# Kernel optimization log

Measured on AMD Instinct MI355X. Metric: run time of the kernel, lower is better.

## Reference

```python
import jax, jax.numpy as jnp
import numpy as np

N, D, E = 16384, 256, 131072  # nodes, feature dim, directed edges (avg sym degree ~16)


def _build_graph(rng):
    # random edges with no self-loops
    r = rng.integers(0, N, E)
    c = (r + 1 + rng.integers(0, N - 1, E)) % N
    e = np.stack([r, c], 1)
    # symmetrize + dedupe + sort == torch sparse coalesce()
    e = np.unique(np.concatenate([e, e[:, ::-1]], 0), axis=0)
    rows, cols = e[:, 0], e[:, 1]
    deg = np.bincount(rows, minlength=N)
    max_deg = int(deg.max())
    off = np.concatenate([[0], np.cumsum(deg)])
    pos = np.arange(rows.shape[0]) - off[rows]
    nbr = np.zeros((N, max_deg), dtype=np.int32)  # padded neighbor lists (CSR rows)
    nbr[rows, pos] = cols
    return nbr, deg.astype(np.int32)


def setup_inputs() -> dict:
    rng = np.random.default_rng(0)
    vertices = jnp.asarray(rng.standard_normal((N, D)).astype(np.float32))
    nbr, deg = _build_graph(rng)
    return {"vertices": vertices, "nbr": jnp.asarray(nbr), "deg": jnp.asarray(deg)}


def _compute_means(vertices, nbr, deg):
    # Sequential greedy edge-based vertex averaging (RelEdgePool phase 1).
    n, d = vertices.shape
    max_deg = nbr.shape[1]
    slot = jnp.arange(max_deg)

    def step(carry, xs):
        unproc, out, c = carry
        i, nbrs_i, deg_i = xs
        valid = slot < deg_i                      # real (non-pad) neighbors
        sel = valid & unproc[nbrs_i]              # unprocessed cluster members (excl. self)
        is_head = unproc[i]                       # vertex starts a new valid cluster
        # mean over unprocessed members; self is always included when head
        s = jnp.einsum('kd,k->d', vertices[nbrs_i], sel.astype(vertices.dtype)) + vertices[i]
        cnt = (jnp.sum(sel) + 1).astype(vertices.dtype)
        mean = s / cnt
        out = out.at[c].set(jnp.where(is_head, mean, out[c]))
        # mark selected members (and self) as processed, only if this is a head
        mark = jnp.zeros(n, bool).at[nbrs_i].max(sel).at[i].set(True)
        unproc = unproc & ~(mark & is_head)
        c = c + is_head.astype(c.dtype)
        return (unproc, out, c), is_head

    init = (jnp.ones(n, dtype=bool), jnp.zeros((n, d), vertices.dtype), jnp.int32(0))
    (_, out, num_clusters), head_mask = jax.lax.scan(
        step, init, (jnp.arange(n), nbr, deg))
    # out[:num_clusters] are the averaged vertices; rows beyond are zero (preallocated buffer,
    # matching the torch code before its final data-dependent slice).
    # head_mask marks vertex_mappings; mean_mappings == arange(num_clusters).
    return out, head_mask, num_clusters


def reference(vertices, nbr, deg):
    return _compute_means(vertices, nbr, deg)
```

## Files before the change

kernel.cpp:

```cpp
#include <hip/hip_runtime.h>
#include <cstdint>
#include <cstddef>

#define NV 16384
#define DD 256
#define TPB 1024
#define BLK 1024
#define PCAP 7
#define HROW 24
#define NPASS 8

#define CFENCE() asm volatile("" ::: "memory")

__global__ __launch_bounds__(256)
void k_prep(const int* __restrict__ nbr, const int* __restrict__ deg,
            int maxdeg, int n, uint4* __restrict__ pend_g,
            unsigned short* __restrict__ hi_g)
{
    int v = blockIdx.x * 256 + threadIdx.x;
    if (v >= n) return;
    const int b  = v & ~(BLK - 1);
    const int dv = deg[v];
    const int* __restrict__ row = nbr + (size_t)v * (size_t)maxdeg;
    unsigned short* __restrict__ hrow = hi_g + (size_t)v * HROW;
    unsigned w0 = 0, w1 = 0, w2 = 0, w3 = 0;
    int cnt = 0, hic = 0;
    for (int k = 0; k < dv; ++k) {
        int j = row[k];
        if (j > v) {
            if (hic < HROW - 1) hrow[1 + hic] = (unsigned short)j;
            ++hic;
        } else if (j >= b) {
            unsigned val = (unsigned)(j - b);
            switch (cnt) {
                case 0: w0 |= val << 16; break;
                case 1: w1 |= val;       break;
                case 2: w1 |= val << 16; break;
                case 3: w2 |= val;       break;
                case 4: w2 |= val << 16; break;
                case 5: w3 |= val;       break;
                case 6: w3 |= val << 16; break;
                default: break;
            }
            ++cnt;
        }
    }
    hrow[0] = (unsigned short)hic;
    w0 |= (unsigned)(cnt > 0xffff ? 0xffff : cnt);
    pend_g[v] = make_uint4(w0, w1, w2, w3);
}

__global__ __launch_bounds__(TPB, 4)
void k_mis(const int* __restrict__ nbr, const int* __restrict__ deg,
           int maxdeg, int n,
           const uint4* __restrict__ pend_g, const unsigned short* __restrict__ hi_g,
           int* __restrict__ headlist, float* __restrict__ out_tail)
{
    __shared__ __align__(16) unsigned char st[NV];
    __shared__ int s_ws[TPB / 64];
    __shared__ int F[3];
    const int t    = threadIdx.x;
    const int lane = t & 63;
    const int wid  = t >> 6;

    ((uint4*)st)[t] = make_uint4(0u, 0u, 0u, 0u);
    if (t < 3) F[t] = 0;
    __syncthreads();

    uint4 pv = make_uint4(0,0,0,0), h0 = pv, h1 = pv, h2 = pv;
    int   dv = 0;
    if (t < n) {
        pv = pend_g[t];
        const uint4* hp = (const uint4*)(hi_g + (size_t)t * HROW);
        h0 = hp[0]; h1 = hp[1]; h2 = hp[2];
        dv = deg[t];
    }
    int r = 0;

    for (int b = 0; b < n; b += BLK) {
        const int v = b + t;
        uint4 pn = make_uint4(0,0,0,0), n0 = pn, n1 = pn, n2 = pn;
        int   dn = 0;
        {
            int vn = b + BLK + t;
            if (vn < n) {
                pn = pend_g[vn];
                const uint4* hp = (const uint4*)(hi_g + (size_t)vn * HROW);
                n0 = hp[0]; n1 = hp[1]; n2 = hp[2];
                dn = deg[vn];
            }
        }

        const int np = pv.x & 0xffff;
        const int e0 = pv.x >> 16,    e1 = pv.y & 0xffff, e2 = pv.y >> 16;
        const int e3 = pv.z & 0xffff, e4 = pv.z >> 16;
        const int e5 = pv.w & 0xffff, e6 = pv.w >> 16;
        const int hic = (int)(h0.x & 0xffff);
        const int* __restrict__ row = nbr + (size_t)v * (size_t)maxdeg;

        int my = (v < n) ? 0 : 2;
        for (;; ++r) {
            if (t == 0) F[(r + 1) % 3] = 0;
            for (int pass = 0; pass < NPASS; ++pass) {
                if (my == 0) {
                    int qv = st[v];
                    int q0 = st[b + e0], q1 = st[b + e1], q2 = st[b + e2];
                    int q3 = st[b + e3], q4 = st[b + e4], q5 = st[b + e5];
                    int q6 = st[b + e6];
                    if (qv != 0) { my = 2; }
                    else {
                        bool anyH = false; int undec = 0;
                        if (np <= PCAP) {
                            if (np > 0) { anyH |= (q0 == 1); undec += (q0 == 0); }
                            if (np > 1) { anyH |= (q1 == 1); undec += (q1 == 0); }
                            if (np > 2) { anyH |= (q2 == 1); undec += (q2 == 0); }
                            if (np > 3) { anyH |= (q3 == 1); undec += (q3 == 0); }
                            if (np > 4) { anyH |= (q4 == 1); undec += (q4 == 0); }
                            if (np > 5) { anyH |= (q5 == 1); undec += (q5 == 0); }
                            if (np > 6) { anyH |= (q6 == 1); undec += (q6 == 0); }
                        } else {
                            for (int k = 0; k < dv; ++k) {
                                int j = row[k];
                                if (j >= b && j < v) {
                                    int q = st[j];
                                    anyH |= (q == 1); undec += (q == 0);
                                }
                            }
                        }
                        if (anyH) { my = 2; st[v] = 2; }
                        else if (undec == 0) {
                            my = 1;
                            st[v] = 1;
                            if (hic <= HROW - 1) {
                                #define PUSHE(word, sh, k) if ((k) < hic) st[((word) >> (sh)) & 0xffffu] = 2
                                PUSHE(h0.x,16, 0); PUSHE(h0.y, 0, 1); PUSHE(h0.y,16, 2);
                                PUSHE(h0.z, 0, 3); PUSHE(h0.z,16, 4); PUSHE(h0.w, 0, 5);
                                PUSHE(h0.w,16, 6);
                                PUSHE(h1.x, 0, 7); PUSHE(h1.x,16, 8); PUSHE(h1.y, 0, 9);
                                PUSHE(h1.y,16,10); PUSHE(h1.z, 0,11); PUSHE(h1.z,16,12);
                                PUSHE(h1.w, 0,13); PUSHE(h1.w,16,14);
                                PUSHE(h2.x, 0,15); PUSHE(h2.x,16,16); PUSHE(h2.y, 0,17);
                                PUSHE(h2.y,16,18); PUSHE(h2.z, 0,19); PUSHE(h2.z,16,20);
                                PUSHE(h2.w, 0,21); PUSHE(h2.w,16,22);
                                #undef PUSHE
                            } else {
                                for (int k = 0; k < dv; ++k) {
                                    int j = row[k];
                                    if (j > v) st[j] = 2;
                                }
                            }
                        }
                    }
                }
                if (__ballot(my == 0) == 0ULL) break;
                CFENCE();
            }
            if (my == 0) F[r % 3] = 1;
            asm volatile("s_waitcnt lgkmcnt(0)\n\ts_barrier" ::: "memory");
            if (F[r % 3] == 0) { ++r; break; }
        }
        pv = pn; h0 = n0; h1 = n1; h2 = n2; dv = dn;
    }

    uint4 qq = ((const uint4*)st)[t];
    int cnt = __popc(qq.x & 0x01010101u) + __popc(qq.y & 0x01010101u)
            + __popc(qq.z & 0x01010101u) + __popc(qq.w & 0x01010101u);
    int c = cnt;
    #pragma unroll
    for (int off = 1; off < 64; off <<= 1) {
        int x = __shfl_up(c, off);
        if (lane >= off) c += x;
    }
    if (lane == 63) s_ws[wid] = c;
    __syncthreads();
    int wexcl = 0, tot = 0;
    #pragma unroll
    for (int w = 0; w < TPB / 64; ++w) {
        int s = s_ws[w];
        tot += s;
        if (w < wid) wexcl += s;
    }
    int excl = wexcl + (c - cnt);
    #pragma unroll
    for (int i = 0; i < 16; ++i) {
        int v = t * 16 + i;
        if (st[v] == 1) { headlist[excl] = v; ++excl; }
    }
    for (int i = t; i < NV / 4; i += TPB) {
        unsigned w = ((const unsigned*)st)[i];
        float4 f;
        f.x = (float)(w & 1u);         f.y = (float)((w >> 8) & 1u);
        f.z = (float)((w >> 16) & 1u); f.w = (float)((w >> 24) & 1u);
        ((float4*)out_tail)[i] = f;
    }
    if (t == 0) out_tail[n] = (float)tot;
}

__global__ __launch_bounds__(256)
void k_avg(const float* __restrict__ vert, const int* __restrict__ nbr,
           const int* __restrict__ deg, int maxdeg, int n,
           const int* __restrict__ headlist,
           const float* __restrict__ tail, float* __restrict__ out)
{
    const int w    = (blockIdx.x * 256 + threadIdx.x) >> 6;
    const int lane = threadIdx.x & 63;
    if (w >= n) return;
    const int tot  = (int)tail[n];
    if (w >= tot) {
        reinterpret_cast<float4*>(out + (size_t)w * DD)[lane] = make_float4(0.f, 0.f, 0.f, 0.f);
        return;
    }
    const int h = headlist[w];

    const int dh = deg[h];
    const int* __restrict__ row = nbr + (size_t)h * (size_t)maxdeg;

    float4 acc = reinterpret_cast<const float4*>(vert + (size_t)h * DD)[lane];
    int cnt = 1;

    for (int k0 = 0; k0 < dh; k0 += 64) {
        int k = k0 + lane;
        int j = (k < dh) ? row[k] : -1;
        bool mem = false;
        if (j > h && tail[j] == 0.0f) {
            const int dj = deg[j];
            const int* __restrict__ rj = nbr + (size_t)j * (size_t)maxdeg;
            int mn = 0x7fffffff;
            for (int kk = 0; kk < dj; ++kk) {
                int u = rj[kk];
                if (tail[u] != 0.0f) mn = min(mn, u);
            }
            mem = (mn == h);
        }
        unsigned long long m = __ballot(mem);
        cnt += __popcll(m);
        while (m) {
            int bit = __ffsll((long long)m) - 1;
            m &= (m - 1);
            int jj = __shfl(j, bit);
            float4 rr = reinterpret_cast<const float4*>(vert + (size_t)jj * DD)[lane];
            acc.x += rr.x; acc.y += rr.y; acc.z += rr.z; acc.w += rr.w;
        }
    }
    const float inv = 1.0f / (float)cnt;
    float4 res;
    res.x = acc.x * inv; res.y = acc.y * inv;
    res.z = acc.z * inv; res.w = acc.w * inv;
    reinterpret_cast<float4*>(out + (size_t)w * DD)[lane] = res;
}

extern "C" void kernel_launch(void* const* d_in, const int* in_sizes, int n_in,
                              void* d_out, int out_size, void* d_ws, size_t ws_size,
                              hipStream_t stream)
{
    const float* vert = (const float*)d_in[0];
    const int*   nbr  = (const int*)d_in[1];
    const int*   deg  = (const int*)d_in[2];

    const int n      = in_sizes[2];
    const int maxdeg = in_sizes[1] / n;
    const int d      = in_sizes[0] / n;

    int*   headlist = (int*)d_ws;
    uint4* pend_g   = (uint4*)(headlist + n);
    unsigned short* hi_g = (unsigned short*)(pend_g + n);

    float* out      = (float*)d_out;
    float* out_tail = out + (size_t)n * (size_t)d;

    hipLaunchKernelGGL(k_prep, dim3((n + 255) / 256), dim3(256), 0, stream,
                       nbr, deg, maxdeg, n, pend_g, hi_g);

    hipLaunchKernelGGL(k_mis, dim3(1), dim3(TPB), 0, stream,
                       nbr, deg, maxdeg, n, pend_g, hi_g, headlist, out_tail);

    const int blocks = (n * 64 + 255) / 256;
    hipLaunchKernelGGL(k_avg, dim3(blocks), dim3(256), 0, stream,
                       vert, nbr, deg, maxdeg, n, headlist, out_tail, out);
}
```

Baseline: 85.55 us.

## Process two vertices per thread with 2048-vertex blocks in MIS sweep

Doubles the block of vertices resolved together, from 1024 to 2048. Each of the 1024 threads now owns two vertices, and the logic is split into decide/do_push helpers. This halves the number of sequential outer blocks and their barrier-synchronised rounds, and the pass count per round is raised from 8 to 12. In exchange, the high-neighbor push lists are loaded from global memory only when a vertex becomes a head, so that load now sits on the critical path. Longer dependency chains inside each bigger block may also need more rounds.

```diff
diff --git a/kernel.cpp b/kernel.cpp
--- a/kernel.cpp
+++ b/kernel.cpp
@@ -5,10 +5,10 @@
 #define NV 16384
 #define DD 256
 #define TPB 1024
-#define BLK 1024
+#define BLK 2048
 #define PCAP 7
 #define HROW 24
-#define NPASS 8
+#define NPASS 12
 
 #define CFENCE() asm volatile("" ::: "memory")
 
@@ -50,6 +50,72 @@
     pend_g[v] = make_uint4(w0, w1, w2, w3);
 }
 
+__device__ __forceinline__
+void do_push(unsigned char* st, int V,
+             const unsigned short* __restrict__ hi_g,
+             const int* __restrict__ nbr, const int* __restrict__ deg,
+             int maxdeg)
+{
+    const uint4* hp = (const uint4*)(hi_g + (size_t)V * HROW);
+    uint4 H0 = hp[0], H1 = hp[1], H2 = hp[2];
+    const int hic = (int)(H0.x & 0xffffu);
+    if (hic <= HROW - 1) {
+        #define PUSHE(word, sh, k) if ((k) < hic) st[((word) >> (sh)) & 0xffffu] = 2
+        PUSHE(H0.x,16, 0); PUSHE(H0.y, 0, 1); PUSHE(H0.y,16, 2);
+        PUSHE(H0.z, 0, 3); PUSHE(H0.z,16, 4); PUSHE(H0.w, 0, 5);
+        PUSHE(H0.w,16, 6);
+        PUSHE(H1.x, 0, 7); PUSHE(H1.x,16, 8); PUSHE(H1.y, 0, 9);
+        PUSHE(H1.y,16,10); PUSHE(H1.z, 0,11); PUSHE(H1.z,16,12);
+        PUSHE(H1.w, 0,13); PUSHE(H1.w,16,14);
+        PUSHE(H2.x, 0,15); PUSHE(H2.x,16,16); PUSHE(H2.y, 0,17);
+        PUSHE(H2.y,16,18); PUSHE(H2.z, 0,19); PUSHE(H2.z,16,20);
+        PUSHE(H2.w, 0,21); PUSHE(H2.w,16,22);
+        #undef PUSHE
+    } else {
+        const int dv = deg[V];
+        const int* __restrict__ row = nbr + (size_t)V * (size_t)maxdeg;
+        for (int k = 0; k < dv; ++k) {
+            int j = row[k];
+            if (j > V) st[j] = 2;
+        }
+    }
+}
+
+__device__ __forceinline__
+void decide(int& my, unsigned char* st, int V, int np, int qown,
+            int q0, int q1, int q2, int q3, int q4, int q5, int q6, int B,
+            const unsigned short* __restrict__ hi_g,
+            const int* __restrict__ nbr, const int* __restrict__ deg,
+            int maxdeg)
+{
+    if (qown != 0) { my = 2; return; }
+    bool anyH = false; int undec = 0;
+    if (np <= PCAP) {
+        if (np > 0) { anyH |= (q0 == 1); undec += (q0 == 0); }
+        if (np > 1) { anyH |= (q1 == 1); undec += (q1 == 0); }
+        if (np > 2) { anyH |= (q2 == 1); undec += (q2 == 0); }
+        if (np > 3) { anyH |= (q3 == 1); undec += (q3 == 0); }
+        if (np > 4) { anyH |= (q4 == 1); undec += (q4 == 0); }
+        if (np > 5) { anyH |= (q5 == 1); undec += (q5 == 0); }
+        if (np > 6) { anyH |= (q6 == 1); undec += (q6 == 0); }
+    } else {
+        const int dv = deg[V];
+        const int* __restrict__ row = nbr + (size_t)V * (size_t)maxdeg;
+        for (int k = 0; k < dv; ++k) {
+            int j = row[k];
+            if (j >= B && j < V) {
+                int q = st[j];
+                anyH |= (q == 1); undec += (q == 0);
+            }
+        }
+    }
+    if (anyH) { my = 2; st[V] = 2; }
+    else if (undec == 0) {
+        my = 1; st[V] = 1;
+        do_push(st, V, hi_g, nbr, deg, maxdeg);
+    }
+}
+
 __global__ __launch_bounds__(TPB, 4)
 void k_mis(const int* __restrict__ nbr, const int* __restrict__ deg,
            int maxdeg, int n,
@@ -67,99 +133,56 @@
     if (t < 3) F[t] = 0;
     __syncthreads();
 
-    uint4 pv = make_uint4(0,0,0,0), h0 = pv, h1 = pv, h2 = pv;
-    int   dv = 0;
-    if (t < n) {
-        pv = pend_g[t];
-        const uint4* hp = (const uint4*)(hi_g + (size_t)t * HROW);
-        h0 = hp[0]; h1 = hp[1]; h2 = hp[2];
-        dv = deg[t];
-    }
+    uint4 pa0 = make_uint4(0,0,0,0), pa1 = pa0;
+    if (t < n)        pa0 = pend_g[t];
+    if (1024 + t < n) pa1 = pend_g[1024 + t];
     int r = 0;
 
     for (int b = 0; b < n; b += BLK) {
-        const int v = b + t;
-        uint4 pn = make_uint4(0,0,0,0), n0 = pn, n1 = pn, n2 = pn;
-        int   dn = 0;
+        const int v0 = b + t, v1 = b + 1024 + t;
+        uint4 qa0 = make_uint4(0,0,0,0), qa1 = qa0;
         {
-            int vn = b + BLK + t;
-            if (vn < n) {
-                pn = pend_g[vn];
-                const uint4* hp = (const uint4*)(hi_g + (size_t)vn * HROW);
-                n0 = hp[0]; n1 = hp[1]; n2 = hp[2];
-                dn = deg[vn];
-            }
-        }
-
-        const int np = pv.x & 0xffff;
-        const int e0 = pv.x >> 16,    e1 = pv.y & 0xffff, e2 = pv.y >> 16;
-        const int e3 = pv.z & 0xffff, e4 = pv.z >> 16;
-        const int e5 = pv.w & 0xffff, e6 = pv.w >> 16;
-        const int hic = (int)(h0.x & 0xffff);
-        const int* __restrict__ row = nbr + (size_t)v * (size_t)maxdeg;
-
-        int my = (v < n) ? 0 : 2;
+            int w0 = b + BLK + t, w1 = b + BLK + 1024 + t;
+            if (w0 < n) qa0 = pend_g[w0];
+            if (w1 < n) qa1 = pend_g[w1];
+        }
+
+        const int np0 = pa0.x & 0xffff;
+        const int e0 = pa0.x >> 16,    e1 = pa0.y & 0xffff, e2 = pa0.y >> 16;
+        const int e3 = pa0.z & 0xffff, e4 = pa0.z >> 16;
+        const int e5 = pa0.w & 0xffff, e6 = pa0.w >> 16;
+        const int np1 = pa1.x & 0xffff;
+        const int f0 = pa1.x >> 16,    f1 = pa1.y & 0xffff, f2 = pa1.y >> 16;
+        const int f3 = pa1.z & 0xffff, f4 = pa1.z >> 16;
+        const int f5 = pa1.w & 0xffff, f6 = pa1.w >> 16;
+
+        int my0 = (v0 < n) ? 0 : 2;
+        int my1 = (v1 < n) ? 0 : 2;
+
         for (;; ++r) {
             if (t == 0) F[(r + 1) % 3] = 0;
             for (int pass = 0; pass < NPASS; ++pass) {
-                if (my == 0) {
-                    int qv = st[v];
-                    int q0 = st[b + e0], q1 = st[b + e1], q2 = st[b + e2];
-                    int q3 = st[b + e3], q4 = st[b + e4], q5 = st[b + e5];
-                    int q6 = st[b + e6];
-                    if (qv != 0) { my = 2; }
-                    else {
-                        bool anyH = false; int undec = 0;
-                        if (np <= PCAP) {
-                            if (np > 0) { anyH |= (q0 == 1); undec += (q0 == 0); }
-                            if (np > 1) { anyH |= (q1 == 1); undec += (q1 == 0); }
-                            if (np > 2) { anyH |= (q2 == 1); undec += (q2 == 0); }
-                            if (np > 3) { anyH |= (q3 == 1); undec += (q3 == 0); }
-                            if (np > 4) { anyH |= (q4 == 1); undec += (q4 == 0); }
-                            if (np > 5) { anyH |= (q5 == 1); undec += (q5 == 0); }
-                            if (np > 6) { anyH |= (q6 == 1); undec += (q6 == 0); }
-                        } else {
-                            for (int k = 0; k < dv; ++k) {
-                                int j = row[k];
-                                if (j >= b && j < v) {
-                                    int q = st[j];
-                                    anyH |= (q == 1); undec += (q == 0);
-                                }
-                            }
-                        }
-                        if (anyH) { my = 2; st[v] = 2; }
-                        else if (undec == 0) {
-                            my = 1;
-                            st[v] = 1;
-                            if (hic <= HROW - 1) {
-                                #define PUSHE(word, sh, k) if ((k) < hic) st[((word) >> (sh)) & 0xffffu] = 2
-                                PUSHE(h0.x,16, 0); PUSHE(h0.y, 0, 1); PUSHE(h0.y,16, 2);
-                                PUSHE(h0.z, 0, 3); PUSHE(h0.z,16, 4); PUSHE(h0.w, 0, 5);
-                                PUSHE(h0.w,16, 6);
-                                PUSHE(h1.x, 0, 7); PUSHE(h1.x,16, 8); PUSHE(h1.y, 0, 9);
-                                PUSHE(h1.y,16,10); PUSHE(h1.z, 0,11); PUSHE(h1.z,16,12);
-                                PUSHE(h1.w, 0,13); PUSHE(h1.w,16,14);
-                                PUSHE(h2.x, 0,15); PUSHE(h2.x,16,16); PUSHE(h2.y, 0,17);
-                                PUSHE(h2.y,16,18); PUSHE(h2.z, 0,19); PUSHE(h2.z,16,20);
-                                PUSHE(h2.w, 0,21); PUSHE(h2.w,16,22);
-                                #undef PUSHE
-                            } else {
-                                for (int k = 0; k < dv; ++k) {
-                                    int j = row[k];
-                                    if (j > v) st[j] = 2;
-                                }
-                            }
-                        }
-                    }
-                }
-                if (__ballot(my == 0) == 0ULL) break;
+                int s0  = st[v0 < n ? v0 : 0],  s1  = st[v1 < n ? v1 : 0];
+                int q00 = st[b + e0], q01 = st[b + e1], q02 = st[b + e2];
+                int q03 = st[b + e3], q04 = st[b + e4], q05 = st[b + e5];
+                int q06 = st[b + e6];
+                int q10 = st[b + f0], q11 = st[b + f1], q12 = st[b + f2];
+                int q13 = st[b + f3], q14 = st[b + f4], q15 = st[b + f5];
+                int q16 = st[b + f6];
+                if (my0 == 0) decide(my0, st, v0, np0, s0,
+                                     q00,q01,q02,q03,q04,q05,q06, b,
+                                     hi_g, nbr, deg, maxdeg);
+                if (my1 == 0) decide(my1, st, v1, np1, s1,
+                                     q10,q11,q12,q13,q14,q15,q16, b,
+                                     hi_g, nbr, deg, maxdeg);
+                if (__ballot((my0 == 0) || (my1 == 0)) == 0ULL) break;
                 CFENCE();
             }
-            if (my == 0) F[r % 3] = 1;
+            if ((my0 == 0) || (my1 == 0)) F[r % 3] = 1;
             asm volatile("s_waitcnt lgkmcnt(0)\n\ts_barrier" ::: "memory");
             if (F[r % 3] == 0) { ++r; break; }
         }
-        pv = pn; h0 = n0; h1 = n1; h2 = n2; dv = dn;
+        pa0 = qa0; pa1 = qa1;
     }
 
     uint4 qq = ((const uint4*)st)[t];
```

New measurement: 87.38 us. 1.02x slower.

## Fuse prep into MIS kernel with per-block flags to overlap preprocessing

Applied to the files above, without the earlier changes.

Merges the preprocessing kernel and the single-block sequential MIS kernel into one launch. Block 0 runs the MIS scan, and the other blocks each preprocess one 1024-vertex chunk and then publish a release flag. The MIS block spin-waits on each chunk's flag before prefetching it, so preprocessing of later chunks overlaps the sequential scan and one kernel launch gap goes away. It adds a memset launch and relies on all blocks being co-resident, with spin-wait overhead on the flags.

```diff
diff --git a/kernel.cpp b/kernel.cpp
--- a/kernel.cpp
+++ b/kernel.cpp
@@ -12,54 +12,74 @@
 
 #define CFENCE() asm volatile("" ::: "memory")
 
-__global__ __launch_bounds__(256)
-void k_prep(const int* __restrict__ nbr, const int* __restrict__ deg,
-            int maxdeg, int n, uint4* __restrict__ pend_g,
-            unsigned short* __restrict__ hi_g)
+__device__ __forceinline__
+void wait_flag(const int* flags, int idx, int lane)
 {
-    int v = blockIdx.x * 256 + threadIdx.x;
-    if (v >= n) return;
-    const int b  = v & ~(BLK - 1);
-    const int dv = deg[v];
-    const int* __restrict__ row = nbr + (size_t)v * (size_t)maxdeg;
-    unsigned short* __restrict__ hrow = hi_g + (size_t)v * HROW;
-    unsigned w0 = 0, w1 = 0, w2 = 0, w3 = 0;
-    int cnt = 0, hic = 0;
-    for (int k = 0; k < dv; ++k) {
-        int j = row[k];
-        if (j > v) {
-            if (hic < HROW - 1) hrow[1 + hic] = (unsigned short)j;
-            ++hic;
-        } else if (j >= b) {
-            unsigned val = (unsigned)(j - b);
-            switch (cnt) {
-                case 0: w0 |= val << 16; break;
-                case 1: w1 |= val;       break;
-                case 2: w1 |= val << 16; break;
-                case 3: w2 |= val;       break;
-                case 4: w2 |= val << 16; break;
-                case 5: w3 |= val;       break;
-                case 6: w3 |= val << 16; break;
-                default: break;
+    for (;;) {
+        int f = 0;
+        if (lane == 0)
+            f = __hip_atomic_load(&flags[idx], __ATOMIC_ACQUIRE,
+                                  __HIP_MEMORY_SCOPE_AGENT);
+        f = __shfl(f, 0);
+        if (f) break;
+        __builtin_amdgcn_s_sleep(1);
+    }
+}
+
+__global__ __launch_bounds__(TPB, 4)
+void k_fused(const int* __restrict__ nbr, const int* __restrict__ deg,
+             int maxdeg, int n,
+             uint4* __restrict__ pend_g, unsigned short* __restrict__ hi_g,
+             int* __restrict__ flags,
+             int* __restrict__ headlist, float* __restrict__ out_tail)
+{
+    const int t = threadIdx.x;
+
+    if (blockIdx.x > 0) {
+        const int r = blockIdx.x - 1;
+        const int v = r * BLK + t;
+        if (v < n) {
+            const int b  = v & ~(BLK - 1);
+            const int dv = deg[v];
+            const int* __restrict__ row = nbr + (size_t)v * (size_t)maxdeg;
+            unsigned short* __restrict__ hrow = hi_g + (size_t)v * HROW;
+            unsigned w0 = 0, w1 = 0, w2 = 0, w3 = 0;
+            int cnt = 0, hic = 0;
+            for (int k = 0; k < dv; ++k) {
+                int j = row[k];
+                if (j > v) {
+                    if (hic < HROW - 1) hrow[1 + hic] = (unsigned short)j;
+                    ++hic;
+                } else if (j >= b) {
+                    unsigned val = (unsigned)(j - b);
+                    switch (cnt) {
+                        case 0: w0 |= val << 16; break;
+                        case 1: w1 |= val;       break;
+                        case 2: w1 |= val << 16; break;
+                        case 3: w2 |= val;       break;
+                        case 4: w2 |= val << 16; break;
+                        case 5: w3 |= val;       break;
+                        case 6: w3 |= val << 16; break;
+                        default: break;
+                    }
+                    ++cnt;
+                }
             }
-            ++cnt;
-        }
-    }
-    hrow[0] = (unsigned short)hic;
-    w0 |= (unsigned)(cnt > 0xffff ? 0xffff : cnt);
-    pend_g[v] = make_uint4(w0, w1, w2, w3);
-}
-
-__global__ __launch_bounds__(TPB, 4)
-void k_mis(const int* __restrict__ nbr, const int* __restrict__ deg,
-           int maxdeg, int n,
-           const uint4* __restrict__ pend_g, const unsigned short* __restrict__ hi_g,
-           int* __restrict__ headlist, float* __restrict__ out_tail)
-{
+            hrow[0] = (unsigned short)hic;
+            w0 |= (unsigned)(cnt > 0xffff ? 0xffff : cnt);
+            pend_g[v] = make_uint4(w0, w1, w2, w3);
+        }
+        __threadfence();
+        __syncthreads();
+        if (t == 0)
+            __hip_atomic_store(&flags[r], 1, __ATOMIC_RELEASE,
+                               __HIP_MEMORY_SCOPE_AGENT);
+        return;
+    }
+
     __shared__ __align__(16) unsigned char st[NV];
     __shared__ int s_ws[TPB / 64];
     __shared__ int F[3];
-    const int t    = threadIdx.x;
     const int lane = t & 63;
     const int wid  = t >> 6;
 
@@ -67,6 +87,7 @@
     if (t < 3) F[t] = 0;
     __syncthreads();
 
+    wait_flag(flags, 0, lane);
     uint4 pv = make_uint4(0,0,0,0), h0 = pv, h1 = pv, h2 = pv;
     int   dv = 0;
     if (t < n) {
@@ -81,7 +102,8 @@
         const int v = b + t;
         uint4 pn = make_uint4(0,0,0,0), n0 = pn, n1 = pn, n2 = pn;
         int   dn = 0;
-        {
+        if (b + BLK < n) {
+            wait_flag(flags, (b + BLK) / BLK, lane);
             int vn = b + BLK + t;
             if (vn < n) {
                 pn = pend_g[vn];
@@ -260,19 +282,21 @@
     const int n      = in_sizes[2];
     const int maxdeg = in_sizes[1] / n;
     const int d      = in_sizes[0] / n;
-
-    int*   headlist = (int*)d_ws;
+    const int nprep  = (n + BLK - 1) / BLK;
+
+    int*   flags    = (int*)d_ws;
+    int*   headlist = flags + 32;
     uint4* pend_g   = (uint4*)(headlist + n);
     unsigned short* hi_g = (unsigned short*)(pend_g + n);
 
     float* out      = (float*)d_out;
     float* out_tail = out + (size_t)n * (size_t)d;
 
-    hipLaunchKernelGGL(k_prep, dim3((n + 255) / 256), dim3(256), 0, stream,
-                       nbr, deg, maxdeg, n, pend_g, hi_g);
-
-    hipLaunchKernelGGL(k_mis, dim3(1), dim3(TPB), 0, stream,
-                       nbr, deg, maxdeg, n, pend_g, hi_g, headlist, out_tail);
+    hipMemsetAsync(flags, 0, 32 * sizeof(int), stream);
+
+    hipLaunchKernelGGL(k_fused, dim3(1 + nprep), dim3(TPB), 0, stream,
+                       nbr, deg, maxdeg, n, pend_g, hi_g, flags,
+                       headlist, out_tail);
 
     const int blocks = (n * 64 + 255) / 256;
     hipLaunchKernelGGL(k_avg, dim3(blocks), dim3(256), 0, stream,
```

New measurement: 135.8 us. 58.7% more time.

## Replace barrier-synchronized block MIS with pull-only spin waiting over lower neighbors

Applied to the files above, without the earlier changes.

The greedy MIS kernel no longer processes 1024-vertex blocks with block-wide barrier rounds and push-style marking of higher neighbors. Each thread now pulls the state of all lower-indexed neighbors (up to 23, packed in a 48-byte record) and spins, per wave, until they are resolved, with a short s_sleep backoff. This relies on vertices being assigned to threads in order and on cross-wave LDS visibility without barriers, which removes round barriers but adds per-wave busy-waiting and a risk of ordering or forward-progress issues. The averaging kernel also stops scanning a neighbor's list at the first head instead of computing the minimum, relying on sorted neighbor lists.

```diff
diff --git a/kernel.cpp b/kernel.cpp
--- a/kernel.cpp
+++ b/kernel.cpp
@@ -5,162 +5,162 @@
 #define NV 16384
 #define DD 256
 #define TPB 1024
-#define BLK 1024
-#define PCAP 7
-#define HROW 24
-#define NPASS 8
+#define NGRP 16
+#define LCAP 23
 
 #define CFENCE() asm volatile("" ::: "memory")
 
 __global__ __launch_bounds__(256)
 void k_prep(const int* __restrict__ nbr, const int* __restrict__ deg,
-            int maxdeg, int n, uint4* __restrict__ pend_g,
-            unsigned short* __restrict__ hi_g)
+            int maxdeg, int n, uint4* __restrict__ pend_g)
 {
     int v = blockIdx.x * 256 + threadIdx.x;
     if (v >= n) return;
-    const int b  = v & ~(BLK - 1);
     const int dv = deg[v];
     const int* __restrict__ row = nbr + (size_t)v * (size_t)maxdeg;
-    unsigned short* __restrict__ hrow = hi_g + (size_t)v * HROW;
-    unsigned w0 = 0, w1 = 0, w2 = 0, w3 = 0;
-    int cnt = 0, hic = 0;
-    for (int k = 0; k < dv; ++k) {
-        int j = row[k];
-        if (j > v) {
-            if (hic < HROW - 1) hrow[1 + hic] = (unsigned short)j;
-            ++hic;
-        } else if (j >= b) {
-            unsigned val = (unsigned)(j - b);
-            switch (cnt) {
-                case 0: w0 |= val << 16; break;
-                case 1: w1 |= val;       break;
-                case 2: w1 |= val << 16; break;
-                case 3: w2 |= val;       break;
-                case 4: w2 |= val << 16; break;
-                case 5: w3 |= val;       break;
-                case 6: w3 |= val << 16; break;
-                default: break;
-            }
-            ++cnt;
-        }
-    }
-    hrow[0] = (unsigned short)hic;
-    w0 |= (unsigned)(cnt > 0xffff ? 0xffff : cnt);
-    pend_g[v] = make_uint4(w0, w1, w2, w3);
+    int nlo = 0;
+    while (nlo < dv && row[nlo] < v) ++nlo;
+
+    unsigned w0=0,w1=0,w2=0,w3=0,w4=0,w5=0,w6=0,w7=0,w8=0,w9=0,w10=0,w11=0;
+    const int m = nlo > LCAP ? LCAP : nlo;
+    for (int i = 0; i < m; ++i) {
+        unsigned e = (unsigned)row[i];
+        switch (i) {
+            case 0:  w0  |= e << 16; break;
+            case 1:  w1  |= e; break;   case 2:  w1  |= e << 16; break;
+            case 3:  w2  |= e; break;   case 4:  w2  |= e << 16; break;
+            case 5:  w3  |= e; break;   case 6:  w3  |= e << 16; break;
+            case 7:  w4  |= e; break;   case 8:  w4  |= e << 16; break;
+            case 9:  w5  |= e; break;   case 10: w5  |= e << 16; break;
+            case 11: w6  |= e; break;   case 12: w6  |= e << 16; break;
+            case 13: w7  |= e; break;   case 14: w7  |= e << 16; break;
+            case 15: w8  |= e; break;   case 16: w8  |= e << 16; break;
+            case 17: w9  |= e; break;   case 18: w9  |= e << 16; break;
+            case 19: w10 |= e; break;   case 20: w10 |= e << 16; break;
+            case 21: w11 |= e; break;   case 22: w11 |= e << 16; break;
+        }
+    }
+    w0 |= (unsigned)(nlo > 0xffff ? 0xffff : nlo);
+    pend_g[3 * (size_t)v]     = make_uint4(w0, w1, w2, w3);
+    pend_g[3 * (size_t)v + 1] = make_uint4(w4, w5, w6, w7);
+    pend_g[3 * (size_t)v + 2] = make_uint4(w8, w9, w10, w11);
 }
 
 __global__ __launch_bounds__(TPB, 4)
 void k_mis(const int* __restrict__ nbr, const int* __restrict__ deg,
-           int maxdeg, int n,
-           const uint4* __restrict__ pend_g, const unsigned short* __restrict__ hi_g,
+           int maxdeg, int n, const uint4* __restrict__ pend_g,
            int* __restrict__ headlist, float* __restrict__ out_tail)
 {
     __shared__ __align__(16) unsigned char st[NV];
     __shared__ int s_ws[TPB / 64];
-    __shared__ int F[3];
     const int t    = threadIdx.x;
     const int lane = t & 63;
     const int wid  = t >> 6;
 
     ((uint4*)st)[t] = make_uint4(0u, 0u, 0u, 0u);
-    if (t < 3) F[t] = 0;
     __syncthreads();
 
-    uint4 pv = make_uint4(0,0,0,0), h0 = pv, h1 = pv, h2 = pv;
-    int   dv = 0;
+    uint4 pa = make_uint4(0,0,0,0), pb = pa, pc = pa;
     if (t < n) {
-        pv = pend_g[t];
-        const uint4* hp = (const uint4*)(hi_g + (size_t)t * HROW);
-        h0 = hp[0]; h1 = hp[1]; h2 = hp[2];
-        dv = deg[t];
-    }
-    int r = 0;
-
-    for (int b = 0; b < n; b += BLK) {
-        const int v = b + t;
-        uint4 pn = make_uint4(0,0,0,0), n0 = pn, n1 = pn, n2 = pn;
-        int   dn = 0;
-        {
-            int vn = b + BLK + t;
+        pa = pend_g[3 * (size_t)t];
+        pb = pend_g[3 * (size_t)t + 1];
+        pc = pend_g[3 * (size_t)t + 2];
+    }
+
+    for (int k = 0; k < NGRP; ++k) {
+        const int v = t + 1024 * k;
+        uint4 qa = make_uint4(0,0,0,0), qb = qa, qc = qa;
+        if (k + 1 < NGRP) {
+            int vn = t + 1024 * (k + 1);
             if (vn < n) {
-                pn = pend_g[vn];
-                const uint4* hp = (const uint4*)(hi_g + (size_t)vn * HROW);
-                n0 = hp[0]; n1 = hp[1]; n2 = hp[2];
-                dn = deg[vn];
+                qa = pend_g[3 * (size_t)vn];
+                qb = pend_g[3 * (size_t)vn + 1];
+                qc = pend_g[3 * (size_t)vn + 2];
             }
         }
 
-        const int np = pv.x & 0xffff;
-        const int e0 = pv.x >> 16,    e1 = pv.y & 0xffff, e2 = pv.y >> 16;
-        const int e3 = pv.z & 0xffff, e4 = pv.z >> 16;
-        const int e5 = pv.w & 0xffff, e6 = pv.w >> 16;
-        const int hic = (int)(h0.x & 0xffff);
+        const int np = (int)(pa.x & 0xffffu);
+        const int e0 = pa.x >> 16;
+        const int e1  = pa.y & 0xffff, e2  = pa.y >> 16;
+        const int e3  = pa.z & 0xffff, e4  = pa.z >> 16;
+        const int e5  = pa.w & 0xffff, e6  = pa.w >> 16;
+        const int e7  = pb.x & 0xffff, e8  = pb.x >> 16;
+        const int e9  = pb.y & 0xffff, e10 = pb.y >> 16;
+        const int e11 = pb.z & 0xffff, e12 = pb.z >> 16;
+        const int e13 = pb.w & 0xffff, e14 = pb.w >> 16;
+        const int e15 = pc.x & 0xffff, e16 = pc.x >> 16;
+        const int e17 = pc.y & 0xffff, e18 = pc.y >> 16;
+        const int e19 = pc.z & 0xffff, e20 = pc.z >> 16;
+        const int e21 = pc.w & 0xffff, e22 = pc.w >> 16;
+
+        int my = (v < n) ? 0 : 2;
+        int dvf = 0;
         const int* __restrict__ row = nbr + (size_t)v * (size_t)maxdeg;
-
-        int my = (v < n) ? 0 : 2;
-        for (;; ++r) {
-            if (t == 0) F[(r + 1) % 3] = 0;
-            for (int pass = 0; pass < NPASS; ++pass) {
+        if (my == 0 && np > LCAP) dvf = deg[v];
+
+        int iter = 0;
+        for (;;) {
+            if (my == 0) {
+                bool anyH = false; int undec = 0;
+                if (np == 0) {
+                    my = 1; st[v] = 1;
+                } else if (np <= LCAP) {
+                    {
+                        int q0=st[e0], q1=st[e1], q2=st[e2], q3=st[e3];
+                        int q4=st[e4], q5=st[e5], q6=st[e6];
+                        if (np > 0) { anyH |= (q0 == 1); undec += (q0 == 0); }
+                        if (np > 1) { anyH |= (q1 == 1); undec += (q1 == 0); }
+                        if (np > 2) { anyH |= (q2 == 1); undec += (q2 == 0); }
+                        if (np > 3) { anyH |= (q3 == 1); undec += (q3 == 0); }
+                        if (np > 4) { anyH |= (q4 == 1); undec += (q4 == 0); }
+                        if (np > 5) { anyH |= (q5 == 1); undec += (q5 == 0); }
+                        if (np > 6) { anyH |= (q6 == 1); undec += (q6 == 0); }
+                    }
+                    if (np > 7) {
+                        int q7=st[e7],  q8=st[e8],  q9=st[e9],  q10=st[e10];
+                        int q11=st[e11], q12=st[e12], q13=st[e13], q14=st[e14];
+                        anyH |= (q7 == 1); undec += (q7 == 0);
+                        if (np > 8)  { anyH |= (q8  == 1); undec += (q8  == 0); }
+                        if (np > 9)  { anyH |= (q9  == 1); undec += (q9  == 0); }
+                        if (np > 10) { anyH |= (q10 == 1); undec += (q10 == 0); }
+                        if (np > 11) { anyH |= (q11 == 1); undec += (q11 == 0); }
+                        if (np > 12) { anyH |= (q12 == 1); undec += (q12 == 0); }
+                        if (np > 13) { anyH |= (q13 == 1); undec += (q13 == 0); }
+                        if (np > 14) { anyH |= (q14 == 1); undec += (q14 == 0); }
+                    }
+                    if (np > 15) {
+                        int q15=st[e15], q16=st[e16], q17=st[e17], q18=st[e18];
+                        int q19=st[e19], q20=st[e20], q21=st[e21], q22=st[e22];
+                        anyH |= (q15 == 1); undec += (q15 == 0);
+                        if (np > 16) { anyH |= (q16 == 1); undec += (q16 == 0); }
+                        if (np > 17) { anyH |= (q17 == 1); undec += (q17 == 0); }
+                        if (np > 18) { anyH |= (q18 == 1); undec += (q18 == 0); }
+                        if (np > 19) { anyH |= (q19 == 1); undec += (q19 == 0); }
+                        if (np > 20) { anyH |= (q20 == 1); undec += (q20 == 0); }
+                        if (np > 21) { anyH |= (q21 == 1); undec += (q21 == 0); }
+                        if (np > 22) { anyH |= (q22 == 1); undec += (q22 == 0); }
+                    }
+                } else {
+                    for (int kk = 0; kk < dvf; ++kk) {
+                        int j = row[kk];
+                        if (j >= v) break;
+                        int q = st[j];
+                        anyH |= (q == 1); undec += (q == 0);
+                    }
+                }
                 if (my == 0) {
-                    int qv = st[v];
-                    int q0 = st[b + e0], q1 = st[b + e1], q2 = st[b + e2];
-                    int q3 = st[b + e3], q4 = st[b + e4], q5 = st[b + e5];
-                    int q6 = st[b + e6];
-                    if (qv != 0) { my = 2; }
-                    else {
-                        bool anyH = false; int undec = 0;
-                        if (np <= PCAP) {
-                            if (np > 0) { anyH |= (q0 == 1); undec += (q0 == 0); }
-                            if (np > 1) { anyH |= (q1 == 1); undec += (q1 == 0); }
-                            if (np > 2) { anyH |= (q2 == 1); undec += (q2 == 0); }
-                            if (np > 3) { anyH |= (q3 == 1); undec += (q3 == 0); }
-                            if (np > 4) { anyH |= (q4 == 1); undec += (q4 == 0); }
-                            if (np > 5) { anyH |= (q5 == 1); undec += (q5 == 0); }
-                            if (np > 6) { anyH |= (q6 == 1); undec += (q6 == 0); }
-                        } else {
-                            for (int k = 0; k < dv; ++k) {
-                                int j = row[k];
-                                if (j >= b && j < v) {
-                                    int q = st[j];
-                                    anyH |= (q == 1); undec += (q == 0);
-                                }
-                            }
-                        }
-                        if (anyH) { my = 2; st[v] = 2; }
-                        else if (undec == 0) {
-                            my = 1;
-                            st[v] = 1;
-                            if (hic <= HROW - 1) {
-                                #define PUSHE(word, sh, k) if ((k) < hic) st[((word) >> (sh)) & 0xffffu] = 2
-                                PUSHE(h0.x,16, 0); PUSHE(h0.y, 0, 1); PUSHE(h0.y,16, 2);
-                                PUSHE(h0.z, 0, 3); PUSHE(h0.z,16, 4); PUSHE(h0.w, 0, 5);
-                                PUSHE(h0.w,16, 6);
-                                PUSHE(h1.x, 0, 7); PUSHE(h1.x,16, 8); PUSHE(h1.y, 0, 9);
-                                PUSHE(h1.y,16,10); PUSHE(h1.z, 0,11); PUSHE(h1.z,16,12);
-                                PUSHE(h1.w, 0,13); PUSHE(h1.w,16,14);
-                                PUSHE(h2.x, 0,15); PUSHE(h2.x,16,16); PUSHE(h2.y, 0,17);
-                                PUSHE(h2.y,16,18); PUSHE(h2.z, 0,19); PUSHE(h2.z,16,20);
-                                PUSHE(h2.w, 0,21); PUSHE(h2.w,16,22);
-                                #undef PUSHE
-                            } else {
-                                for (int k = 0; k < dv; ++k) {
-                                    int j = row[k];
-                                    if (j > v) st[j] = 2;
-                                }
-                            }
-                        }
-                    }
+                    if (anyH)            { my = 2; st[v] = 2; }
+                    else if (undec == 0) { my = 1; st[v] = 1; }
                 }
-                if (__ballot(my == 0) == 0ULL) break;
-                CFENCE();
             }
-            if (my == 0) F[r % 3] = 1;
-            asm volatile("s_waitcnt lgkmcnt(0)\n\ts_barrier" ::: "memory");
-            if (F[r % 3] == 0) { ++r; break; }
-        }
-        pv = pn; h0 = n0; h1 = n1; h2 = n2; dv = dn;
-    }
+            if (__ballot(my == 0) == 0ULL) break;
+            CFENCE();
+            if (iter++ > 0) __builtin_amdgcn_s_sleep(1);
+        }
+        pa = qa; pb = qb; pc = qc;
+    }
+
+    __syncthreads();
 
     uint4 qq = ((const uint4*)st)[t];
     int cnt = __popc(qq.x & 0x01010101u) + __popc(qq.y & 0x01010101u)
@@ -225,12 +225,10 @@
         if (j > h && tail[j] == 0.0f) {
             const int dj = deg[j];
             const int* __restrict__ rj = nbr + (size_t)j * (size_t)maxdeg;
-            int mn = 0x7fffffff;
             for (int kk = 0; kk < dj; ++kk) {
                 int u = rj[kk];
-                if (tail[u] != 0.0f) mn = min(mn, u);
+                if (tail[u] != 0.0f) { mem = (u == h); break; }
             }
-            mem = (mn == h);
         }
         unsigned long long m = __ballot(mem);
         cnt += __popcll(m);
@@ -263,16 +261,15 @@
 
     int*   headlist = (int*)d_ws;
     uint4* pend_g   = (uint4*)(headlist + n);
-    unsigned short* hi_g = (unsigned short*)(pend_g + n);
 
     float* out      = (float*)d_out;
     float* out_tail = out + (size_t)n * (size_t)d;
 
     hipLaunchKernelGGL(k_prep, dim3((n + 255) / 256), dim3(256), 0, stream,
-                       nbr, deg, maxdeg, n, pend_g, hi_g);
+                       nbr, deg, maxdeg, n, pend_g);
 
     hipLaunchKernelGGL(k_mis, dim3(1), dim3(TPB), 0, stream,
-                       nbr, deg, maxdeg, n, pend_g, hi_g, headlist, out_tail);
+                       nbr, deg, maxdeg, n, pend_g, headlist, out_tail);
 
     const int blocks = (n * 64 + 255) / 256;
     hipLaunchKernelGGL(k_avg, dim3(blocks), dim3(256), 0, stream,
```

After: 87.94 us. 2.8% more time.
